# Kernel optimization log

Measured on AMD Instinct MI355X. Metric: run time of the kernel, lower is better.

The kernel has to match this reference:

```python
import jax, jax.numpy as jnp
import numpy as np

N, NFEAT, NHID, NCLASS, NHEADS = 8192, 512, 64, 16, 4
ALPHA = 0.2          # leaky_relu slope for attention scores
OUT_SLOPE = 0.01     # flax default slope for per-head output leaky_relu
NEG = -9000000000000000.0


def glorot(key, shape):
    fan_in, fan_out = shape[0], shape[1]
    lim = jnp.sqrt(6.0 / (fan_in + fan_out))
    return jax.random.uniform(key, shape, jnp.float32, -lim, lim)


def setup_inputs() -> dict:
    key = jax.random.key(0)
    ks = jax.random.split(key, 6)
    x = jax.random.normal(ks[0], (N, NFEAT), jnp.float32)
    adj = jax.random.randint(ks[1], (N, N), 0, 2, jnp.int32)
    Wh = glorot(ks[2], (NHEADS * NFEAT, NHID)).reshape(NHEADS, NFEAT, NHID)
    ah = glorot(ks[3], (NHEADS * 2 * NHID, 1)).reshape(NHEADS, 2 * NHID, 1)
    Wo = glorot(ks[4], (NHID * NHEADS, NCLASS))
    ao = glorot(ks[5], (2 * NCLASS, 1))
    return {"x": x, "adj": adj, "Wh": Wh, "ah": ah, "Wo": Wo, "ao": ao}


def _gat_layer(x, adj_mask, W, a, score_slope):
    # h: (N, F)
    h = x @ W
    F = h.shape[1]
    # a_input[i,j] = concat(h_i, h_j); a_input @ a == f1[i] + f2[j]
    f1 = h @ a[:F, 0]   # (N,)
    f2 = h @ a[F:, 0]   # (N,)
    e = jax.nn.leaky_relu(f1[:, None] + f2[None, :], negative_slope=score_slope)
    att = jax.nn.softmax(jnp.where(adj_mask, e, NEG), axis=1)  # (N, N)
    return att @ h  # (N, F)


def reference(x, adj, Wh, ah, Wo, ao):
    adj_mask = adj > 0
    heads = []
    for k in range(NHEADS):  # small fixed structural loop
        hp = _gat_layer(x, adj_mask, Wh[k], ah[k], ALPHA)
        heads.append(jax.nn.leaky_relu(hp, negative_slope=OUT_SLOPE))
    xcat = jnp.concatenate(heads, axis=1)  # (N, NHEADS*NHID)
    # output head: concat=False -> return h_prime directly
    return _gat_layer(xcat, adj_mask, Wo, ao, ALPHA)  # (N, NCLASS)
```

## Files before the change

### kernel.cpp

```cpp
#include <hip/hip_runtime.h>
#include <stdint.h>

#define N      8192
#define FEAT   512
#define HID    64
#define NH     4
#define C1     256
#define PCH    80
#define TC     320
#define NCLS   16
#define C2     32
#define IPB    8
#define LOG2E  1.44269504f

typedef __attribute__((ext_vector_type(8))) short bf16x8;
typedef __attribute__((ext_vector_type(4))) float f32x4;

__device__ __forceinline__ float b2f(uint16_t u){
  uint32_t x = ((uint32_t)u) << 16;
  return __builtin_bit_cast(float, x);
}
__device__ __forceinline__ uint16_t f2b(float f){
  uint32_t x = __builtin_bit_cast(uint32_t, f);
  uint32_t r = (x + 0x7fffu + ((x >> 16) & 1u)) >> 16;
  return (uint16_t)r;
}
__device__ __forceinline__ float lrelu(float v, float a){ return fmaxf(v, a * v); }
__device__ __forceinline__ float fexp2(float x){
#if __has_builtin(__builtin_amdgcn_exp2f)
  return __builtin_amdgcn_exp2f(x);
#else
  return exp2f(x);
#endif
}
__device__ __forceinline__ uint32_t pk_bf16(float lo, float hi){
  uint32_t r;
  asm("v_cvt_pk_bf16_f32 %0, %1, %2" : "=v"(r) : "v"(lo), "v"(hi));
  return r;
}

__global__ void k0_wht(const float* __restrict__ Wh, float* __restrict__ WhT){
  int idx = blockIdx.x * 256 + threadIdx.x;
  int k = idx >> 15;
  int r = idx & 32767;
  int cc = r >> 9, f = r & 511;
  WhT[idx] = Wh[k * 32768 + f * 64 + cc];
}

__global__ __launch_bounds__(256) void k1_h(const float* __restrict__ x,
    const float* __restrict__ WhT, const float* __restrict__ ah,
    uint16_t* __restrict__ H, float* __restrict__ f1, float* __restrict__ f2)
{
  __shared__ float4 xs[IPB][128];
  int t = threadIdx.x;
  int i0 = blockIdx.x * IPB;
  for (int r = t; r < IPB * 128; r += 256){
    int ii = r >> 7, o = r & 127;
    xs[ii][o] = *((const float4*)(x + (size_t)(i0 + ii) * FEAT) + o);
  }
  __syncthreads();
  int k = t >> 6, cc = t & 63;
  const float4* wrow = (const float4*)(WhT + k * 32768 + cc * 512);
  float acc[IPB] = {};
  for (int f4 = 0; f4 < 128; ++f4){
    float4 wv = wrow[f4];
    #pragma unroll
    for (int ii = 0; ii < IPB; ++ii){
      float4 xv = xs[ii][f4];
      acc[ii] += xv.x * wv.x + xv.y * wv.y + xv.z * wv.z + xv.w * wv.w;
    }
  }
  float a1 = ah[k * 128 + cc], a2 = ah[k * 128 + 64 + cc];
  #pragma unroll
  for (int ii = 0; ii < IPB; ++ii){
    int i = i0 + ii;
    H[(size_t)i * C1 + t] = f2b(acc[ii]);
    float c1v = acc[ii] * a1, c2v = acc[ii] * a2;
    #pragma unroll
    for (int off = 32; off; off >>= 1){
      c1v += __shfl_down(c1v, off);
      c2v += __shfl_down(c2v, off);
    }
    if (cc == 0){ f1[k * N + i] = c1v * LOG2E; f2[k * N + i] = c2v * LOG2E; }
  }
}

__global__ void k2a_htT(const uint16_t* __restrict__ H, uint16_t* __restrict__ HT){
  __shared__ uint16_t tile[64][65];
  int bid = blockIdx.x;
  int k = bid & 3, it = bid >> 2;
  int i0 = it * 64;
  int t = threadIdx.x;
  #pragma unroll
  for (int r = 0; r < 4; ++r){
    int ii = r * 16 + (t >> 4);
    int pp = (t & 15) * 4;
    uint2 v = *(const uint2*)(H + (size_t)(i0 + ii) * C1 + k * 64 + pp);
    const uint16_t* s = (const uint16_t*)&v;
    tile[pp + 0][ii] = s[0]; tile[pp + 1][ii] = s[1];
    tile[pp + 2][ii] = s[2]; tile[pp + 3][ii] = s[3];
  }
  __syncthreads();
  #pragma unroll
  for (int r = 0; r < 4; ++r){
    int pp = r * 16 + (t >> 4);
    int ii = (t & 15) * 4;
    uint2 v;
    uint16_t* s = (uint16_t*)&v;
    s[0] = tile[pp][ii + 0]; s[1] = tile[pp][ii + 1];
    s[2] = tile[pp][ii + 2]; s[3] = tile[pp][ii + 3];
    *(uint2*)(HT + (size_t)k * (64 * N) + (size_t)pp * N + i0 + ii) = v;
  }
}

#define K3_BODY(JC, CUR, NXT)                                                    \
  {                                                                              \
    __syncthreads();                                                             \
    *(uint4*)&Hl[p0][o40 * 8] = h##CUR##0;                                       \
    *(uint4*)&Hl[p1][o40 * 8] = h##CUR##1;                                       \
    const int gjn = js * 2048 + (((JC) + 1) & 63) * 32;                          \
    h##NXT##0 = *(const uint4*)(src0 + gjn);                                     \
    h##NXT##1 = *(const uint4*)(src1 + gjn);                                     \
    _Pragma("unroll")                                                            \
    for (int r = 0; r < 4; ++r) av##NXT[r] = arow[(size_t)(16 * r) * N + gjn];   \
    _Pragma("unroll")                                                            \
    for (int k = 0; k < 4; ++k) f##NXT[k] = f2[(size_t)k * N + gjn + tj];        \
    _Pragma("unroll")                                                            \
    for (int r = 0; r < 4; ++r){                                                 \
      const int i = half + 16 * r;                                               \
      const int a = av##CUR[r];                                                  \
      float e0, e1, e2, e3;                                                      \
      { float s = f1s[0][i] + f##CUR[0]; e0 = fexp2(fmaxf(s, 0.2f * s)); }       \
      { float s = f1s[1][i] + f##CUR[1]; e1 = fexp2(fmaxf(s, 0.2f * s)); }       \
      { float s = f1s[2][i] + f##CUR[2]; e2 = fexp2(fmaxf(s, 0.2f * s)); }       \
      { float s = f1s[3][i] + f##CUR[3]; e3 = fexp2(fmaxf(s, 0.2f * s)); }       \
      if (a <= 0){ e0 = 0.f; e1 = 0.f; e2 = 0.f; e3 = 0.f; }                     \
      dsum[0][r] += e0; dsum[1][r] += e1;                                        \
      dsum[2][r] += e2; dsum[3][r] += e3;                                        \
      uint32_t pk01 = pk_bf16(e0, e1), pk23 = pk_bf16(e2, e3);                   \
      Pl[0][i][tj] = (uint16_t)pk01; Pl[1][i][tj] = (uint16_t)(pk01 >> 16);      \
      Pl[2][i][tj] = (uint16_t)pk23; Pl[3][i][tj] = (uint16_t)(pk23 >> 16);      \
    }                                                                            \
    __syncthreads();                                                             \
    bf16x8 af0 = *(const bf16x8*)&Pl[head][(ith * 2 + 0) * 16 + m][q * 8];       \
    bf16x8 af1 = *(const bf16x8*)&Pl[head][(ith * 2 + 1) * 16 + m][q * 8];       \
    _Pragma("unroll")                                                            \
    for (int ct = 0; ct < 4; ++ct){                                              \
      bf16x8 bfr = *(const bf16x8*)&Hl[head * 64 + ct * 16 + m][q * 8];          \
      acc[0][ct] = __builtin_amdgcn_mfma_f32_16x16x32_bf16(af0, bfr, acc[0][ct], 0, 0, 0); \
      acc[1][ct] = __builtin_amdgcn_mfma_f32_16x16x32_bf16(af1, bfr, acc[1][ct], 0, 0, 0); \
    }                                                                            \
  }

__global__ __launch_bounds__(512, 4) void k3_attA(const int* __restrict__ adj,
    const uint16_t* __restrict__ HT, const float* __restrict__ f1,
    const float* __restrict__ f2, float* __restrict__ accA)
{
  __shared__ uint16_t Pl[NH][64][40];
  __shared__ uint16_t Hl[256][40];
  __shared__ float f1s[NH][64];

  const int t = threadIdx.x;
  const int ibl = blockIdx.x >> 2;
  const int js = blockIdx.x & 3;
  const int gi0 = ibl * 64;

  if (t < 256){ int k = t >> 6, ii = t & 63; f1s[k][ii] = f1[k * N + gi0 + ii]; }

  const int tj   = t & 31;
  const int half = t >> 5;
  const int lane = t & 63;
  const int w    = t >> 6;
  const int head = w >> 1;
  const int ith  = w & 1;
  const int m    = lane & 15;
  const int q    = lane >> 4;

  const int p0 = t >> 2, o40 = t & 3;
  const int p1 = p0 + 128;
  const uint16_t* src0 = HT + (size_t)p0 * N + o40 * 8;
  const uint16_t* src1 = HT + (size_t)p1 * N + o40 * 8;

  f32x4 acc[2][4] = {};
  float dsum[NH][4] = {};
  const int* arow = adj + (size_t)(gi0 + half) * N + tj;

  uint4 hA0, hA1, hB0, hB1;
  int avA[4], avB[4];
  float fA[4], fB[4];

  {
    const int gj0 = js * 2048;
    hA0 = *(const uint4*)(src0 + gj0);
    hA1 = *(const uint4*)(src1 + gj0);
    #pragma unroll
    for (int r = 0; r < 4; ++r) avA[r] = arow[(size_t)(16 * r) * N + gj0];
    #pragma unroll
    for (int k = 0; k < 4; ++k) fA[k] = f2[(size_t)k * N + gj0 + tj];
  }

  for (int jc = 0; jc < 64; jc += 2){
    K3_BODY(jc,     A, B)
    K3_BODY(jc + 1, B, A)
  }

  #pragma unroll
  for (int itl = 0; itl < 2; ++itl)
    #pragma unroll
    for (int ct = 0; ct < 4; ++ct)
      #pragma unroll
      for (int reg = 0; reg < 4; ++reg){
        int gi = gi0 + (ith * 2 + itl) * 16 + q * 4 + reg;
        accA[((size_t)js * N + gi) * TC + head * PCH + ct * 16 + m] = acc[itl][ct][reg];
      }
  #pragma unroll
  for (int k = 0; k < 4; ++k)
    #pragma unroll
    for (int r = 0; r < 4; ++r){
      float v = dsum[k][r];
      v += __shfl_xor(v, 16);
      v += __shfl_xor(v, 8);
      v += __shfl_xor(v, 4);
      v += __shfl_xor(v, 2);
      v += __shfl_xor(v, 1);
      if (tj == 0)
        accA[((size_t)js * N + gi0 + half + 16 * r) * TC + k * PCH + 64] = v;
    }
}

__global__ void k4_redA(const float* __restrict__ accA, uint16_t* __restrict__ xcat){
  int i = blockIdx.x;
  int t = threadIdx.x;
  int k = t >> 6, cc = t & 63;
  size_t base = (size_t)i * TC + k * PCH;
  float v = 0.f, Z = 0.f;
  #pragma unroll
  for (int js = 0; js < 4; ++js){
    const float* p = accA + (size_t)js * N * TC + base;
    v += p[cc];
    Z += p[64];
  }
  float r = v / Z;
  xcat[(size_t)i * C1 + t] = f2b(lrelu(r, 0.01f));
}

__global__ __launch_bounds__(256) void k5_h2(const uint16_t* __restrict__ xcat,
    const float* __restrict__ Wo, const float* __restrict__ ao,
    uint16_t* __restrict__ h2T, float* __restrict__ f1o, float* __restrict__ f2o)
{
  __shared__ uint16_t xs[16][256];
  int t = threadIdx.x;
  int i0 = blockIdx.x * 16;
  #pragma unroll
  for (int r = 0; r < 2; ++r){
    int idx = t + 256 * r;
    int ii = idx >> 5, o4 = idx & 31;
    *(uint4*)&xs[ii][o4 * 8] = *(const uint4*)(xcat + (size_t)(i0 + ii) * C1 + o4 * 8);
  }
  __syncthreads();
  int ii = t >> 4, c = t & 15;
  float acc = 0.f;
  for (int f = 0; f < 256; ++f)
    acc += b2f(xs[ii][f]) * Wo[f * 16 + c];
  int i = i0 + ii;
  h2T[(size_t)c * N + i] = f2b(acc);
  float u1 = acc * ao[c];
  float u2 = acc * ao[16 + c];
  #pragma unroll
  for (int off = 8; off; off >>= 1){
    u1 += __shfl_down(u1, off, 16);
    u2 += __shfl_down(u2, off, 16);
  }
  if (c == 0){ f1o[i] = u1 * LOG2E; f2o[i] = u2 * LOG2E; }
}

#define K6_BODY(JC, CUR, NXT)                                                    \
  {                                                                              \
    __syncthreads();                                                             \
    if (stg) *(uint4*)&Hl[p0][o40 * 8] = h##CUR;                                 \
    const int gjn = js * 1024 + (((JC) + 1) & 31) * 32;                          \
    if (stg) h##NXT = *(const uint4*)(h2T + (size_t)p0 * N + gjn + o40 * 8);     \
    _Pragma("unroll")                                                            \
    for (int r = 0; r < 8; ++r) av##NXT[r] = arow[(size_t)(8 * r) * N + gjn];    \
    f##NXT = f2o[gjn + tj];                                                      \
    _Pragma("unroll")                                                            \
    for (int rr = 0; rr < 4; ++rr){                                              \
      const int i0r = half + 16 * rr;                                            \
      const int i1r = i0r + 8;                                                   \
      float s0 = f1s[i0r] + f##CUR;                                              \
      float s1 = f1s[i1r] + f##CUR;                                              \
      float e0 = fexp2(fmaxf(s0, 0.2f * s0));                                    \
      float e1 = fexp2(fmaxf(s1, 0.2f * s1));                                    \
      if (av##CUR[2 * rr]     <= 0) e0 = 0.f;                                    \
      if (av##CUR[2 * rr + 1] <= 0) e1 = 0.f;                                    \
      dsum[2 * rr] += e0; dsum[2 * rr + 1] += e1;                                \
      uint32_t pk = pk_bf16(e0, e1);                                             \
      Pl[i0r][tj] = (uint16_t)pk; Pl[i1r][tj] = (uint16_t)(pk >> 16);            \
    }                                                                            \
    __syncthreads();                                                             \
    bf16x8 af = *(const bf16x8*)&Pl[wid * 16 + m][q * 8];                        \
    bf16x8 b0 = *(const bf16x8*)&Hl[m][q * 8];                                   \
    acc0 = __builtin_amdgcn_mfma_f32_16x16x32_bf16(af, b0, acc0, 0, 0, 0);       \
  }

__global__ __launch_bounds__(256) void k6_attB(const int* __restrict__ adj,
    const uint16_t* __restrict__ h2T, const float* __restrict__ f1o,
    const float* __restrict__ f2o, float* __restrict__ accB)
{
  __shared__ uint16_t Pl[64][40];
  __shared__ uint16_t Hl[16][40];
  __shared__ float f1s[64];

  const int t = threadIdx.x;
  const int ibl = blockIdx.x >> 3;
  const int js = blockIdx.x & 7;
  const int gi0 = ibl * 64;
  if (t < 64) f1s[t] = f1o[gi0 + t];

  const int tj = t & 31;
  const int half = t >> 5;
  const int lane = t & 63;
  const int wid = t >> 6;
  const int m = lane & 15;
  const int q = lane >> 4;

  const int p0 = t >> 2, o40 = t & 3;
  const bool stg = (t < 64);

  f32x4 acc0 = {0.f, 0.f, 0.f, 0.f};
  float dsum[8] = {};
  const int* arow = adj + (size_t)(gi0 + half) * N + tj;

  uint4 hA = {}, hB = {};
  int avA[8], avB[8];
  float fA, fB;

  {
    const int gj0 = js * 1024;
    if (stg) hA = *(const uint4*)(h2T + (size_t)p0 * N + gj0 + o40 * 8);
    #pragma unroll
    for (int r = 0; r < 8; ++r) avA[r] = arow[(size_t)(8 * r) * N + gj0];
    fA = f2o[gj0 + tj];
  }

  for (int jc = 0; jc < 32; jc += 2){
    K6_BODY(jc,     A, B)
    K6_BODY(jc + 1, B, A)
  }

  #pragma unroll
  for (int reg = 0; reg < 4; ++reg){
    int gi = gi0 + wid * 16 + q * 4 + reg;
    accB[((size_t)js * N + gi) * C2 + m] = acc0[reg];
  }
  #pragma unroll
  for (int r = 0; r < 8; ++r){
    float v = dsum[r];
    v += __shfl_xor(v, 16);
    v += __shfl_xor(v, 8);
    v += __shfl_xor(v, 4);
    v += __shfl_xor(v, 2);
    v += __shfl_xor(v, 1);
    if (tj == 0)
      accB[((size_t)js * N + gi0 + half + 8 * r) * C2 + 16] = v;
  }
}

__global__ void k7_redB(const float* __restrict__ accB, float* __restrict__ out){
  int idx = blockIdx.x * 256 + threadIdx.x;
  int i = idx >> 4, c = idx & 15;
  float v = 0.f, Z = 0.f;
  #pragma unroll
  for (int js = 0; js < 8; ++js){
    const float* p = accB + ((size_t)js * N + i) * C2;
    v += p[c];
    Z += p[16];
  }
  out[idx] = v / Z;
}

extern "C" void kernel_launch(void* const* d_in, const int* in_sizes, int n_in,
                              void* d_out, int out_size, void* d_ws, size_t ws_size,
                              hipStream_t stream)
{
  const float* x   = (const float*)d_in[0];
  const int*   adj = (const int*)d_in[1];
  const float* Wh  = (const float*)d_in[2];
  const float* ah  = (const float*)d_in[3];
  const float* Wo  = (const float*)d_in[4];
  const float* ao  = (const float*)d_in[5];
  float* out = (float*)d_out;

  char* ws = (char*)d_ws;
  float*    WhT  = (float*)   (ws);
  uint16_t* H    = (uint16_t*)(ws + 524288);
  uint16_t* HT   = (uint16_t*)(ws + 4718592);
  float*    f1   = (float*)   (ws + 8912896);
  float*    f2   = (float*)   (ws + 9043968);
  float*    accA = (float*)   (ws + 9175040);
  uint16_t* xcat = (uint16_t*)(ws + 51118080);
  uint16_t* h2T  = (uint16_t*)(ws + 55312384);
  float*    f1o  = (float*)   (ws + 55574528);
  float*    f2o  = (float*)   (ws + 55607296);
  float*    accB = (float*)   (ws + 55640064);

  hipLaunchKernelGGL(k0_wht,   dim3(512),  dim3(256), 0, stream, Wh, WhT);
  hipLaunchKernelGGL(k1_h,     dim3(1024), dim3(256), 0, stream, x, WhT, ah, H, f1, f2);
  hipLaunchKernelGGL(k2a_htT,  dim3(512),  dim3(256), 0, stream, H, HT);
  hipLaunchKernelGGL(k3_attA,  dim3(512),  dim3(512), 0, stream, adj, HT, f1, f2, accA);
  hipLaunchKernelGGL(k4_redA,  dim3(8192), dim3(256), 0, stream, accA, xcat);
  hipLaunchKernelGGL(k5_h2,    dim3(512),  dim3(256), 0, stream, xcat, Wo, ao, h2T, f1o, f2o);
  hipLaunchKernelGGL(k6_attB,  dim3(1024), dim3(256), 0, stream, adj, h2T, f1o, f2o, accB);
  hipLaunchKernelGGL(k7_redB,  dim3(512),  dim3(256), 0, stream, accB, out);
}
```

Before: 587.1 us.

## Bit-pack adjacency and build MFMA A-fragments directly in registers

Adds a pre-pass that packs the int32 adjacency matrix into a bitmask with wave ballots, so the two attention kernels read 32 neighbours per 32-bit word instead of 32 int loads. The attention kernels now compute exp scores directly in the MFMA A-operand layout per lane, which removes the P tile in LDS and one barrier per step. They also double-buffer the H tile in LDS. The packing kernel still reads the full 256 MB adjacency once, but this replaces two full reads in the attention kernels. The change also shrinks the padded accA layout.

Result: slower. 615.1 us (+4.8%).

```diff
diff --git a/kernel.cpp b/kernel.cpp
--- a/kernel.cpp
+++ b/kernel.cpp
@@ -2,12 +2,13 @@
 #include <stdint.h>
 
 #define N      8192
+#define NW32   256
 #define FEAT   512
 #define HID    64
 #define NH     4
 #define C1     256
-#define PCH    80
-#define TC     320
+#define PCH    65
+#define TC     260
 #define NCLS   16
 #define C2     32
 #define IPB    8
@@ -37,6 +38,39 @@
   uint32_t r;
   asm("v_cvt_pk_bf16_f32 %0, %1, %2" : "=v"(r) : "v"(lo), "v"(hi));
   return r;
+}
+
+__device__ __forceinline__ bf16x8 mk_frag(float f1v, float4 fa, float4 fb,
+                                          uint32_t ub, float& dsum){
+  float e0, e1, e2, e3, e4, e5, e6, e7, s;
+  s = f1v + fa.x; e0 = fexp2(fmaxf(s, 0.2f * s)); if (!(ub &   1u)) e0 = 0.f;
+  s = f1v + fa.y; e1 = fexp2(fmaxf(s, 0.2f * s)); if (!(ub &   2u)) e1 = 0.f;
+  s = f1v + fa.z; e2 = fexp2(fmaxf(s, 0.2f * s)); if (!(ub &   4u)) e2 = 0.f;
+  s = f1v + fa.w; e3 = fexp2(fmaxf(s, 0.2f * s)); if (!(ub &   8u)) e3 = 0.f;
+  s = f1v + fb.x; e4 = fexp2(fmaxf(s, 0.2f * s)); if (!(ub &  16u)) e4 = 0.f;
+  s = f1v + fb.y; e5 = fexp2(fmaxf(s, 0.2f * s)); if (!(ub &  32u)) e5 = 0.f;
+  s = f1v + fb.z; e6 = fexp2(fmaxf(s, 0.2f * s)); if (!(ub &  64u)) e6 = 0.f;
+  s = f1v + fb.w; e7 = fexp2(fmaxf(s, 0.2f * s)); if (!(ub & 128u)) e7 = 0.f;
+  dsum += ((e0 + e1) + (e2 + e3)) + ((e4 + e5) + (e6 + e7));
+  union { uint32_t u[4]; bf16x8 v; } r;
+  r.u[0] = pk_bf16(e0, e1);
+  r.u[1] = pk_bf16(e2, e3);
+  r.u[2] = pk_bf16(e4, e5);
+  r.u[3] = pk_bf16(e6, e7);
+  return r.v;
+}
+
+__global__ __launch_bounds__(256) void kp_pack(const int* __restrict__ adj,
+                                               unsigned long long* __restrict__ adjP64){
+  int t = threadIdx.x;
+  int lane = t & 63;
+  int wg = blockIdx.x * 4 + (t >> 6);
+  for (int it = 0; it < 128; ++it){
+    size_t c = (size_t)it * 8192 + wg;
+    int v = adj[c * 64 + lane];
+    unsigned long long m = __ballot(v > 0);
+    if (lane == 0) adjP64[c] = m;
+  }
 }
 
 __global__ void k0_wht(const float* __restrict__ Wh, float* __restrict__ WhT){
@@ -113,62 +147,41 @@
   }
 }
 
-#define K3_BODY(JC, CUR, NXT)                                                    \
-  {                                                                              \
-    __syncthreads();                                                             \
-    *(uint4*)&Hl[p0][o40 * 8] = h##CUR##0;                                       \
-    *(uint4*)&Hl[p1][o40 * 8] = h##CUR##1;                                       \
-    const int gjn = js * 2048 + (((JC) + 1) & 63) * 32;                          \
-    h##NXT##0 = *(const uint4*)(src0 + gjn);                                     \
-    h##NXT##1 = *(const uint4*)(src1 + gjn);                                     \
-    _Pragma("unroll")                                                            \
-    for (int r = 0; r < 4; ++r) av##NXT[r] = arow[(size_t)(16 * r) * N + gjn];   \
-    _Pragma("unroll")                                                            \
-    for (int k = 0; k < 4; ++k) f##NXT[k] = f2[(size_t)k * N + gjn + tj];        \
-    _Pragma("unroll")                                                            \
-    for (int r = 0; r < 4; ++r){                                                 \
-      const int i = half + 16 * r;                                               \
-      const int a = av##CUR[r];                                                  \
-      float e0, e1, e2, e3;                                                      \
-      { float s = f1s[0][i] + f##CUR[0]; e0 = fexp2(fmaxf(s, 0.2f * s)); }       \
-      { float s = f1s[1][i] + f##CUR[1]; e1 = fexp2(fmaxf(s, 0.2f * s)); }       \
-      { float s = f1s[2][i] + f##CUR[2]; e2 = fexp2(fmaxf(s, 0.2f * s)); }       \
-      { float s = f1s[3][i] + f##CUR[3]; e3 = fexp2(fmaxf(s, 0.2f * s)); }       \
-      if (a <= 0){ e0 = 0.f; e1 = 0.f; e2 = 0.f; e3 = 0.f; }                     \
-      dsum[0][r] += e0; dsum[1][r] += e1;                                        \
-      dsum[2][r] += e2; dsum[3][r] += e3;                                        \
-      uint32_t pk01 = pk_bf16(e0, e1), pk23 = pk_bf16(e2, e3);                   \
-      Pl[0][i][tj] = (uint16_t)pk01; Pl[1][i][tj] = (uint16_t)(pk01 >> 16);      \
-      Pl[2][i][tj] = (uint16_t)pk23; Pl[3][i][tj] = (uint16_t)(pk23 >> 16);      \
-    }                                                                            \
-    __syncthreads();                                                             \
-    bf16x8 af0 = *(const bf16x8*)&Pl[head][(ith * 2 + 0) * 16 + m][q * 8];       \
-    bf16x8 af1 = *(const bf16x8*)&Pl[head][(ith * 2 + 1) * 16 + m][q * 8];       \
-    _Pragma("unroll")                                                            \
-    for (int ct = 0; ct < 4; ++ct){                                              \
-      bf16x8 bfr = *(const bf16x8*)&Hl[head * 64 + ct * 16 + m][q * 8];          \
+#define K3_BODY(JC, CUR, NXT)                                                   \
+  {                                                                             \
+    *(uint4*)&Hl[(JC) & 1][p0][o40 * 8] = h##CUR##0;                            \
+    *(uint4*)&Hl[(JC) & 1][p1][o40 * 8] = h##CUR##1;                            \
+    const int gjn = js * 2048 + (((JC) + 1) & 63) * 32;                         \
+    h##NXT##0 = *(const uint4*)(src0 + gjn);                                    \
+    h##NXT##1 = *(const uint4*)(src1 + gjn);                                    \
+    w##NXT##0 = adjP[arow0 + (gjn >> 5)];                                       \
+    w##NXT##1 = adjP[arow1 + (gjn >> 5)];                                       \
+    f##NXT##0 = *(const float4*)(f2h + gjn + 8 * q);                            \
+    f##NXT##1 = *(const float4*)(f2h + gjn + 8 * q + 4);                        \
+    bf16x8 af0 = mk_frag(f1v0, f##CUR##0, f##CUR##1,                            \
+                         (w##CUR##0 >> (8 * q)) & 255u, dsum0);                 \
+    bf16x8 af1 = mk_frag(f1v1, f##CUR##0, f##CUR##1,                            \
+                         (w##CUR##1 >> (8 * q)) & 255u, dsum1);                 \
+    __syncthreads();                                                            \
+    _Pragma("unroll")                                                           \
+    for (int ct = 0; ct < 4; ++ct){                                             \
+      bf16x8 bfr = *(const bf16x8*)&Hl[(JC) & 1][head * 64 + ct * 16 + m][q * 8]; \
       acc[0][ct] = __builtin_amdgcn_mfma_f32_16x16x32_bf16(af0, bfr, acc[0][ct], 0, 0, 0); \
       acc[1][ct] = __builtin_amdgcn_mfma_f32_16x16x32_bf16(af1, bfr, acc[1][ct], 0, 0, 0); \
-    }                                                                            \
-  }
-
-__global__ __launch_bounds__(512, 4) void k3_attA(const int* __restrict__ adj,
+    }                                                                           \
+  }
+
+__global__ __launch_bounds__(512, 4) void k3_attA(const uint32_t* __restrict__ adjP,
     const uint16_t* __restrict__ HT, const float* __restrict__ f1,
     const float* __restrict__ f2, float* __restrict__ accA)
 {
-  __shared__ uint16_t Pl[NH][64][40];
-  __shared__ uint16_t Hl[256][40];
-  __shared__ float f1s[NH][64];
+  __shared__ uint16_t Hl[2][256][40];
 
   const int t = threadIdx.x;
   const int ibl = blockIdx.x >> 2;
   const int js = blockIdx.x & 3;
   const int gi0 = ibl * 64;
 
-  if (t < 256){ int k = t >> 6, ii = t & 63; f1s[k][ii] = f1[k * N + gi0 + ii]; }
-
-  const int tj   = t & 31;
-  const int half = t >> 5;
   const int lane = t & 63;
   const int w    = t >> 6;
   const int head = w >> 1;
@@ -181,22 +194,28 @@
   const uint16_t* src0 = HT + (size_t)p0 * N + o40 * 8;
   const uint16_t* src1 = HT + (size_t)p1 * N + o40 * 8;
 
+  const int row0 = gi0 + ith * 32 + m;
+  const int arow0 = row0 * NW32;
+  const int arow1 = (row0 + 16) * NW32;
+  const float* f2h = f2 + (size_t)head * N;
+  const float f1v0 = f1[(size_t)head * N + row0];
+  const float f1v1 = f1[(size_t)head * N + row0 + 16];
+
   f32x4 acc[2][4] = {};
-  float dsum[NH][4] = {};
-  const int* arow = adj + (size_t)(gi0 + half) * N + tj;
+  float dsum0 = 0.f, dsum1 = 0.f;
 
   uint4 hA0, hA1, hB0, hB1;
-  int avA[4], avB[4];
-  float fA[4], fB[4];
+  uint32_t wA0, wA1, wB0, wB1;
+  float4 fA0, fA1, fB0, fB1;
 
   {
     const int gj0 = js * 2048;
     hA0 = *(const uint4*)(src0 + gj0);
     hA1 = *(const uint4*)(src1 + gj0);
-    #pragma unroll
-    for (int r = 0; r < 4; ++r) avA[r] = arow[(size_t)(16 * r) * N + gj0];
-    #pragma unroll
-    for (int k = 0; k < 4; ++k) fA[k] = f2[(size_t)k * N + gj0 + tj];
+    wA0 = adjP[arow0 + (gj0 >> 5)];
+    wA1 = adjP[arow1 + (gj0 >> 5)];
+    fA0 = *(const float4*)(f2h + gj0 + 8 * q);
+    fA1 = *(const float4*)(f2h + gj0 + 8 * q + 4);
   }
 
   for (int jc = 0; jc < 64; jc += 2){
@@ -210,22 +229,18 @@
     for (int ct = 0; ct < 4; ++ct)
       #pragma unroll
       for (int reg = 0; reg < 4; ++reg){
-        int gi = gi0 + (ith * 2 + itl) * 16 + q * 4 + reg;
+        int gi = gi0 + ith * 32 + itl * 16 + q * 4 + reg;
         accA[((size_t)js * N + gi) * TC + head * PCH + ct * 16 + m] = acc[itl][ct][reg];
       }
-  #pragma unroll
-  for (int k = 0; k < 4; ++k)
-    #pragma unroll
-    for (int r = 0; r < 4; ++r){
-      float v = dsum[k][r];
-      v += __shfl_xor(v, 16);
-      v += __shfl_xor(v, 8);
-      v += __shfl_xor(v, 4);
-      v += __shfl_xor(v, 2);
-      v += __shfl_xor(v, 1);
-      if (tj == 0)
-        accA[((size_t)js * N + gi0 + half + 16 * r) * TC + k * PCH + 64] = v;
+  {
+    float v0 = dsum0, v1 = dsum1;
+    v0 += __shfl_xor(v0, 16); v0 += __shfl_xor(v0, 32);
+    v1 += __shfl_xor(v1, 16); v1 += __shfl_xor(v1, 32);
+    if (q == 0){
+      accA[((size_t)js * N + row0)      * TC + head * PCH + 64] = v0;
+      accA[((size_t)js * N + row0 + 16) * TC + head * PCH + 64] = v1;
     }
+  }
 }
 
 __global__ void k4_redA(const float* __restrict__ accA, uint16_t* __restrict__ xcat){
@@ -274,73 +289,57 @@
   if (c == 0){ f1o[i] = u1 * LOG2E; f2o[i] = u2 * LOG2E; }
 }
 
-#define K6_BODY(JC, CUR, NXT)                                                    \
-  {                                                                              \
-    __syncthreads();                                                             \
-    if (stg) *(uint4*)&Hl[p0][o40 * 8] = h##CUR;                                 \
-    const int gjn = js * 1024 + (((JC) + 1) & 31) * 32;                          \
-    if (stg) h##NXT = *(const uint4*)(h2T + (size_t)p0 * N + gjn + o40 * 8);     \
-    _Pragma("unroll")                                                            \
-    for (int r = 0; r < 8; ++r) av##NXT[r] = arow[(size_t)(8 * r) * N + gjn];    \
-    f##NXT = f2o[gjn + tj];                                                      \
-    _Pragma("unroll")                                                            \
-    for (int rr = 0; rr < 4; ++rr){                                              \
-      const int i0r = half + 16 * rr;                                            \
-      const int i1r = i0r + 8;                                                   \
-      float s0 = f1s[i0r] + f##CUR;                                              \
-      float s1 = f1s[i1r] + f##CUR;                                              \
-      float e0 = fexp2(fmaxf(s0, 0.2f * s0));                                    \
-      float e1 = fexp2(fmaxf(s1, 0.2f * s1));                                    \
-      if (av##CUR[2 * rr]     <= 0) e0 = 0.f;                                    \
-      if (av##CUR[2 * rr + 1] <= 0) e1 = 0.f;                                    \
-      dsum[2 * rr] += e0; dsum[2 * rr + 1] += e1;                                \
-      uint32_t pk = pk_bf16(e0, e1);                                             \
-      Pl[i0r][tj] = (uint16_t)pk; Pl[i1r][tj] = (uint16_t)(pk >> 16);            \
-    }                                                                            \
-    __syncthreads();                                                             \
-    bf16x8 af = *(const bf16x8*)&Pl[wid * 16 + m][q * 8];                        \
-    bf16x8 b0 = *(const bf16x8*)&Hl[m][q * 8];                                   \
-    acc0 = __builtin_amdgcn_mfma_f32_16x16x32_bf16(af, b0, acc0, 0, 0, 0);       \
-  }
-
-__global__ __launch_bounds__(256) void k6_attB(const int* __restrict__ adj,
+#define K6_BODY(JC, CUR, NXT)                                                   \
+  {                                                                             \
+    if (stg) *(uint4*)&Hl[(JC) & 1][p0][o40 * 8] = h##CUR;                      \
+    const int gjn = js * 1024 + (((JC) + 1) & 31) * 32;                         \
+    if (stg) h##NXT = *(const uint4*)(h2T + (size_t)p0 * N + gjn + o40 * 8);    \
+    w##NXT = adjP[arow + (gjn >> 5)];                                           \
+    f##NXT##0 = *(const float4*)(f2o + gjn + 8 * q);                            \
+    f##NXT##1 = *(const float4*)(f2o + gjn + 8 * q + 4);                        \
+    bf16x8 af = mk_frag(f1v, f##CUR##0, f##CUR##1,                              \
+                        (w##CUR >> (8 * q)) & 255u, dsum);                      \
+    __syncthreads();                                                            \
+    bf16x8 b0 = *(const bf16x8*)&Hl[(JC) & 1][m][q * 8];                        \
+    acc0 = __builtin_amdgcn_mfma_f32_16x16x32_bf16(af, b0, acc0, 0, 0, 0);      \
+  }
+
+__global__ __launch_bounds__(256) void k6_attB(const uint32_t* __restrict__ adjP,
     const uint16_t* __restrict__ h2T, const float* __restrict__ f1o,
     const float* __restrict__ f2o, float* __restrict__ accB)
 {
-  __shared__ uint16_t Pl[64][40];
-  __shared__ uint16_t Hl[16][40];
-  __shared__ float f1s[64];
+  __shared__ uint16_t Hl[2][16][40];
 
   const int t = threadIdx.x;
   const int ibl = blockIdx.x >> 3;
   const int js = blockIdx.x & 7;
   const int gi0 = ibl * 64;
-  if (t < 64) f1s[t] = f1o[gi0 + t];
-
-  const int tj = t & 31;
-  const int half = t >> 5;
+
   const int lane = t & 63;
-  const int wid = t >> 6;
+  const int w = t >> 6;
   const int m = lane & 15;
   const int q = lane >> 4;
 
   const int p0 = t >> 2, o40 = t & 3;
   const bool stg = (t < 64);
 
+  const int row = gi0 + w * 16 + m;
+  const int arow = row * NW32;
+  const float f1v = f1o[row];
+
   f32x4 acc0 = {0.f, 0.f, 0.f, 0.f};
-  float dsum[8] = {};
-  const int* arow = adj + (size_t)(gi0 + half) * N + tj;
+  float dsum = 0.f;
 
   uint4 hA = {}, hB = {};
-  int avA[8], avB[8];
-  float fA, fB;
+  uint32_t wA, wB;
+  float4 fA0, fA1, fB0, fB1;
 
   {
     const int gj0 = js * 1024;
     if (stg) hA = *(const uint4*)(h2T + (size_t)p0 * N + gj0 + o40 * 8);
-    #pragma unroll
-    for (int r = 0; r < 8; ++r) avA[r] = arow[(size_t)(8 * r) * N + gj0];
-    fA = f2o[gj0 + tj];
+    wA = adjP[arow + (gj0 >> 5)];
+    fA0 = *(const float4*)(f2o + gj0 + 8 * q);
+    fA1 = *(const float4*)(f2o + gj0 + 8 * q + 4);
   }
 
   for (int jc = 0; jc < 32; jc += 2){
@@ -350,19 +349,14 @@
 
   #pragma unroll
   for (int reg = 0; reg < 4; ++reg){
-    int gi = gi0 + wid * 16 + q * 4 + reg;
+    int gi = gi0 + w * 16 + q * 4 + reg;
     accB[((size_t)js * N + gi) * C2 + m] = acc0[reg];
   }
-  #pragma unroll
-  for (int r = 0; r < 8; ++r){
-    float v = dsum[r];
-    v += __shfl_xor(v, 16);
-    v += __shfl_xor(v, 8);
-    v += __shfl_xor(v, 4);
-    v += __shfl_xor(v, 2);
-    v += __shfl_xor(v, 1);
-    if (tj == 0)
-      accB[((size_t)js * N + gi0 + half + 8 * r) * C2 + 16] = v;
+  {
+    float v = dsum;
+    v += __shfl_xor(v, 16); v += __shfl_xor(v, 32);
+    if (q == 0)
+      accB[((size_t)js * N + row) * C2 + 16] = v;
   }
 }
 
@@ -398,18 +392,20 @@
   float*    f1   = (float*)   (ws + 8912896);
   float*    f2   = (float*)   (ws + 9043968);
   float*    accA = (float*)   (ws + 9175040);
-  uint16_t* xcat = (uint16_t*)(ws + 51118080);
-  uint16_t* h2T  = (uint16_t*)(ws + 55312384);
-  float*    f1o  = (float*)   (ws + 55574528);
-  float*    f2o  = (float*)   (ws + 55607296);
-  float*    accB = (float*)   (ws + 55640064);
-
+  uint16_t* xcat = (uint16_t*)(ws + 43253760);
+  uint16_t* h2T  = (uint16_t*)(ws + 47448064);
+  float*    f1o  = (float*)   (ws + 47710208);
+  float*    f2o  = (float*)   (ws + 47742976);
+  float*    accB = (float*)   (ws + 47775744);
+  void*     adjP = (void*)    (ws + 56164352);
+
+  hipLaunchKernelGGL(kp_pack,  dim3(2048), dim3(256), 0, stream, adj, (unsigned long long*)adjP);
   hipLaunchKernelGGL(k0_wht,   dim3(512),  dim3(256), 0, stream, Wh, WhT);
   hipLaunchKernelGGL(k1_h,     dim3(1024), dim3(256), 0, stream, x, WhT, ah, H, f1, f2);
   hipLaunchKernelGGL(k2a_htT,  dim3(512),  dim3(256), 0, stream, H, HT);
-  hipLaunchKernelGGL(k3_attA,  dim3(512),  dim3(512), 0, stream, adj, HT, f1, f2, accA);
+  hipLaunchKernelGGL(k3_attA,  dim3(512),  dim3(512), 0, stream, (const uint32_t*)adjP, HT, f1, f2, accA);
   hipLaunchKernelGGL(k4_redA,  dim3(8192), dim3(256), 0, stream, accA, xcat);
   hipLaunchKernelGGL(k5_h2,    dim3(512),  dim3(256), 0, stream, xcat, Wo, ao, h2T, f1o, f2o);
-  hipLaunchKernelGGL(k6_attB,  dim3(1024), dim3(256), 0, stream, adj, h2T, f1o, f2o, accB);
+  hipLaunchKernelGGL(k6_attB,  dim3(1024), dim3(256), 0, stream, (const uint32_t*)adjP, h2T, f1o, f2o, accB);
   hipLaunchKernelGGL(k7_redB,  dim3(512),  dim3(256), 0, stream, accB, out);
 }
```
